# Performance work log

Hardware: AMD Instinct MI355X
Metric: run time of the kernel (lower is better)

Reference implementation:

```python
import jax, jax.numpy as jnp
import numpy as np

NEG_SLOPE = 0.01  # nn.LeakyReLU default
N_NODES = 38332
POI_LEN = 38333
CAT_LEN = 400
POI_DIM = 300
CAT_DIM = 100
GCN_CH = 64
GCN_LAYERS = 5
N_EDGES = N_NODES * 32


def leaky(x):
    return jnp.where(x >= 0, x, NEG_SLOPE * x)


def gcn_conv(x, src, dst, W, b):
    """PyG GCNConv: add self loops + symmetric normalization.
    out = D^-1/2 (A+I) D^-1/2 X W + b, deg computed with self loops."""
    n = x.shape[0]
    h = x @ W  # [N, out]
    deg = jax.ops.segment_sum(jnp.ones_like(dst, dtype=h.dtype), dst, num_segments=n) + 1.0
    dinv = jax.lax.rsqrt(deg)  # deg >= 1 always (self loop)
    norm = dinv[src] * dinv[dst]  # [E]
    agg = jax.ops.segment_sum(h[src] * norm[:, None], dst, num_segments=n)
    agg = agg + h * (1.0 / deg)[:, None]  # self-loop term: norm_ii = 1/deg_i
    return agg + b


def setup_inputs() -> dict:
    key = jax.random.key(0)
    ks = jax.random.split(key, 16)
    poi_ids = jax.random.randint(ks[0], (N_NODES, 1), 0, POI_LEN).astype(jnp.float32)
    cat_ids = jax.random.randint(ks[1], (N_NODES, 1), 0, CAT_LEN).astype(jnp.float32)
    feats = jax.random.normal(ks[2], (N_NODES, 3), dtype=jnp.float32)
    x = jnp.concatenate([poi_ids, cat_ids, feats], axis=1)  # [N,5]
    edge_index = jax.random.randint(ks[3], (2, N_EDGES), 0, N_NODES, dtype=jnp.int32)

    def glorot(k, shape):
        lim = float(np.sqrt(6.0 / (shape[0] + shape[1])))
        return jax.random.uniform(k, shape, jnp.float32, -lim, lim)

    d_in = POI_DIM + CAT_DIM + 3  # 403
    params = {
        "poi_emb": jax.random.normal(ks[4], (POI_LEN, POI_DIM), jnp.float32),
        "cat_emb": jax.random.normal(ks[5], (CAT_LEN, CAT_DIM), jnp.float32),
        "W_in": glorot(ks[6], (d_in, GCN_CH)),
        "b_in": jnp.zeros((GCN_CH,), jnp.float32),
        "gcn_Ws": jnp.stack([glorot(jax.random.fold_in(ks[7], i), (GCN_CH, GCN_CH)) for i in range(GCN_LAYERS)]),
        "gcn_bs": jnp.zeros((GCN_LAYERS, GCN_CH), jnp.float32),
        "W_out": glorot(ks[8], (GCN_CH, 1)),
        "b_out": jnp.zeros((1,), jnp.float32),
        "fc1_W": glorot(ks[9], (N_NODES, 128)),
        "fc1_b": jnp.zeros((128,), jnp.float32),
        "fc2_W": glorot(ks[10], (128, POI_LEN)),
        "fc2_b": jnpos if False else jnp.zeros((POI_LEN,), jnp.float32),
    }
    return {"x": x, "edge_index": edge_index, **params}


def reference(x, edge_index, poi_emb, cat_emb, W_in, b_in, gcn_Ws, gcn_bs, W_out, b_out, fc1_W, fc1_b, fc2_W, fc2_b):
    src, dst = edge_index[0], edge_index[1]
    poi_f = poi_emb[x[:, 0].astype(jnp.int32)]  # [N,300]
    cat_f = cat_emb[x[:, 1].astype(jnp.int32)]  # [N,100]
    feat = jnp.concatenate([poi_f, cat_f, x[:, 2:5]], axis=1)  # [N,403]
    feat = leaky(gcn_conv(feat, src, dst, W_in, b_in))
    for i in range(GCN_LAYERS):
        t = gcn_conv(feat, src, dst, gcn_Ws[i], gcn_bs[i])
        feat = leaky(t) + t  # GcnUnit: relu(temp) + temp
    feat = leaky(gcn_conv(feat, src, dst, W_out, b_out)).reshape(-1)  # [N]
    h = jax.nn.relu(feat @ fc1_W + fc1_b)
    out = jax.nn.relu(h @ fc2_W + fc2_b)  # [poi_len]
    return out
```

## Files before the change

### kernel.cpp

```cpp
#include <hip/hip_runtime.h>
#include <hip/hip_bf16.h>

#define N_NODES 38332
#define POI_LEN 38333
#define CAT_LEN 400
#define POI_DIM 300
#define CAT_DIM 100
#define N_EDGES (N_NODES * 32)
#define NEG_SLOPE 0.01f
#define B1 ((N_NODES + 127) / 128)
#define SPLIT_CHUNK 2048
#define NSPLIT ((N_EDGES + SPLIT_CHUNK - 1) / SPLIT_CHUNK)
#define PLACE_CAP 8192
#define BCAP 8192

typedef __attribute__((ext_vector_type(8))) short short8;
typedef __attribute__((ext_vector_type(4))) float f32x4;

__device__ __forceinline__ unsigned short f2bf(float f) {
  unsigned u = __float_as_uint(f);
  u += 0x7fff + ((u >> 16) & 1);
  return (unsigned short)(u >> 16);
}
__device__ __forceinline__ float bflo(unsigned u) {
  return __uint_as_float(u << 16);
}
__device__ __forceinline__ float bfhi(unsigned u) {
  return __uint_as_float(u & 0xffff0000u);
}


#define WFIN_ELEMS (13 * 2048)
#define WFGCN_ELEMS (5 * 4096)

__global__ __launch_bounds__(256) void k_prep(const float* __restrict__ W_in,
                                              const float* __restrict__ gcn_Ws,
                                              unsigned short* __restrict__ wf_in,
                                              unsigned short* __restrict__ wf_gcn,
                                              int* __restrict__ bcnt,
                                              float* __restrict__ h128) {
  int idx = blockIdx.x * 256 + threadIdx.x;
  if (idx < B1) bcnt[idx] = 0;
  if (idx < 128) h128[idx] = 0.f;
  if (idx < WFIN_ELEMS) {
    int j = idx & 7, n = (idx >> 3) & 63, q = (idx >> 9) & 3, ks = idx >> 11;
    int k = ks * 32 + q * 8 + j;
    wf_in[idx] = f2bf((k < 400) ? W_in[k * 64 + n] : 0.f);
  } else if (idx < WFIN_ELEMS + WFGCN_ELEMS) {
    int t = idx - WFIN_ELEMS;
    int l = t >> 12, i = t & 4095;
    int j = i & 7, n = (i >> 3) & 63, q = (i >> 9) & 3, ks = i >> 11;
    int k = ks * 32 + q * 8 + j;
    wf_gcn[t] = f2bf(gcn_Ws[(size_t)l * 4096 + k * 64 + n]);
  }
}


__global__ __launch_bounds__(256) void k_split(const int* __restrict__ src,
                                               const int* __restrict__ dst,
                                               int* __restrict__ bcnt,
                                               int* __restrict__ staging) {
  __shared__ int hist[B1];
  __shared__ int lbase[B1];
  __shared__ int lcur[B1];
  int tid = threadIdx.x;
  int base = blockIdx.x * SPLIT_CHUNK;
  int n = N_EDGES - base;
  if (n > SPLIT_CHUNK) n = SPLIT_CHUNK;
  for (int b = tid; b < B1; b += 256) {
    hist[b] = 0;
    lcur[b] = 0;
  }
  __syncthreads();
  for (int i = tid; i < n; i += 256) atomicAdd(&hist[dst[base + i] >> 7], 1);
  __syncthreads();
  for (int b = tid; b < B1; b += 256) {
    int c = hist[b];
    lbase[b] = c ? atomicAdd(&bcnt[b], c) : 0;
  }
  __syncthreads();
  for (int i = tid; i < n; i += 256) {
    int d = dst[base + i];
    int s = src[base + i];
    int b = d >> 7;
    int off = atomicAdd(&lcur[b], 1);
    staging[(size_t)b * BCAP + lbase[b] + off] = (s << 7) | (d & 127);
  }
}

__global__ __launch_bounds__(256) void k_place(const int* __restrict__ staging,
                                               const int* __restrict__ bcnt,
                                               int* __restrict__ csr_src,
                                               int2* __restrict__ rs,
                                               float* __restrict__ dinv) {
  __shared__ int lc[128];
  __shared__ int ls[256];
  __shared__ int cur[128];
  __shared__ int buf[PLACE_CAP];
  int b = blockIdx.x;
  int tid = threadIdx.x;
  int d0 = b * 128;
  int nd = N_NODES - d0;
  if (nd > 128) nd = 128;
  int cnt_b = bcnt[b];
  const int* st = staging + (size_t)b * BCAP;
  if (tid < 128) lc[tid] = 0;
  __syncthreads();
  for (int i = tid; i < cnt_b; i += 256) atomicAdd(&lc[st[i] & 127], 1);
  __syncthreads();
  int v = (tid < 128) ? lc[tid] : 0;
  ls[tid] = v;
  __syncthreads();
  for (int off = 1; off < 128; off <<= 1) {
    int t = (tid >= off) ? ls[tid - off] : 0;
    __syncthreads();
    ls[tid] += t;
    __syncthreads();
  }
  if (tid < 128) {
    int excl = ls[tid] - v;
    cur[tid] = excl;
    if (tid < nd) {
      rs[d0 + tid] = make_int2(b * BCAP + excl, v);
      dinv[d0 + tid] = 1.0f / sqrtf((float)(v + 1));
    }
  }
  __syncthreads();
  for (int i = tid; i < cnt_b; i += 256) {
    int p = st[i];
    int pos = atomicAdd(&cur[p & 127], 1);
    buf[pos] = p >> 7;
  }
  __syncthreads();
  int base = b * BCAP;
  for (int i = tid; i < cnt_b; i += 256) csr_src[base + i] = buf[i];
}


__global__ __launch_bounds__(256) void k_front(
    const float* __restrict__ x, const float* __restrict__ poi_emb,
    const float* __restrict__ cat_emb, const float* __restrict__ W_in,
    const unsigned short* __restrict__ wf_in, const float* __restrict__ dinv,
    unsigned short* __restrict__ hs) {
  constexpr int KP = 416, RS = 424, NK4 = 104;
  __shared__ unsigned short sA[16 * RS];
  __shared__ float sC[16 * 68];
  __shared__ int sPid[16], sCid[16];
  __shared__ float sX[16][3];
  int tid = threadIdx.x;
  int row0 = blockIdx.x * 16;
  if (tid < 16) {
    int row = row0 + tid;
    if (row < N_NODES) {
      sPid[tid] = (int)x[row * 5 + 0];
      sCid[tid] = (int)x[row * 5 + 1];
      sX[tid][0] = x[row * 5 + 2];
      sX[tid][1] = x[row * 5 + 3];
      sX[tid][2] = x[row * 5 + 4];
    } else {
      sPid[tid] = 0; sCid[tid] = 0;
      sX[tid][0] = sX[tid][1] = sX[tid][2] = 0.f;
    }
  }
  __syncthreads();
  for (int idx = tid; idx < 16 * NK4; idx += 256) {
    int r = idx / NK4;
    int k = (idx - r * NK4) * 4;
    ushort4 o = {0, 0, 0, 0};
    if (k < 400 && row0 + r < N_NODES) {
      float4 f;
      if (k < 300) f = *(const float4*)(poi_emb + (size_t)sPid[r] * 300 + k);
      else         f = *(const float4*)(cat_emb + (size_t)sCid[r] * 100 + (k - 300));
      o.x = f2bf(f.x); o.y = f2bf(f.y); o.z = f2bf(f.z); o.w = f2bf(f.w);
    }
    *(ushort4*)&sA[r * RS + k] = o;
  }
  __syncthreads();
  int lane = tid & 63, wv = tid >> 6;
  int c = lane & 15, q = lane >> 4, n0 = wv * 16;
  f32x4 acc = {0.f, 0.f, 0.f, 0.f};
  const unsigned short* arow = &sA[c * RS];
#pragma unroll
  for (int ks = 0; ks < KP / 32; ks++) {
    short8 af = *(const short8*)(arow + ks * 32 + q * 8);
    short8 bf = *(const short8*)(wf_in + ((size_t)((ks * 4 + q) * 64 + n0 + c)) * 8);
    acc = __builtin_amdgcn_mfma_f32_16x16x32_bf16(af, bf, acc, 0, 0, 0);
  }
#pragma unroll
  for (int r = 0; r < 4; r++) sC[(q * 4 + r) * 68 + n0 + c] = acc[r];
  __syncthreads();
  for (int idx = tid; idx < 16 * 64; idx += 256) {
    int r = idx >> 6, col = idx & 63;
    int row = row0 + r;
    if (row < N_NODES) {
      float v = sC[r * 68 + col] + sX[r][0] * W_in[400 * 64 + col] +
                sX[r][1] * W_in[401 * 64 + col] + sX[r][2] * W_in[402 * 64 + col];
      hs[(size_t)row * 64 + col] = f2bf(v * dinv[row]);
    }
  }
}


template <int MODE>
__global__ __launch_bounds__(256) void k_agg(const unsigned short* __restrict__ hs,
                                             const int2* __restrict__ rs,
                                             const int* __restrict__ csr_src,
                                             const float* __restrict__ dinv,
                                             const float* __restrict__ bias,
                                             const unsigned short* __restrict__ Wf,
                                             unsigned short* __restrict__ hs_next,
                                             const float* __restrict__ W_out,
                                             float* __restrict__ hs1) {
  __shared__ unsigned short sA[16 * 72];
  __shared__ float sC[4 * 68];
  int tid = threadIdx.x;
  int lane = tid & 63;
  int wv = tid >> 6;
  int node = blockIdx.x * 4 + wv;
  int eslot = lane >> 3;
  int ch8 = lane & 7;
  if (MODE != 2) {
    for (int i = tid; i < 216; i += 256)
      *(ushort4*)&sA[288 + i * 4] = (ushort4){0, 0, 0, 0};
  }
  int2 rr = rs[node];
  int r0 = rr.x, r1 = rr.x + rr.y;
  float4 a0 = {0.f, 0.f, 0.f, 0.f}, a1 = a0;
#define ACC8(v)                                                              \
  do {                                                                       \
    a0.x += bflo((v).x); a0.y += bfhi((v).x);                                \
    a0.z += bflo((v).y); a0.w += bfhi((v).y);                                \
    a1.x += bflo((v).z); a1.y += bfhi((v).z);                                \
    a1.z += bflo((v).w); a1.w += bfhi((v).w);                                \
  } while (0)
  int e = r0 + eslot;
  for (; e + 24 < r1; e += 32) {
    int s0 = csr_src[e];
    int s1 = csr_src[e + 8];
    int s2 = csr_src[e + 16];
    int s3 = csr_src[e + 24];
    uint4 v0 = *(const uint4*)(hs + (size_t)s0 * 64 + ch8 * 8);
    uint4 v1 = *(const uint4*)(hs + (size_t)s1 * 64 + ch8 * 8);
    uint4 v2 = *(const uint4*)(hs + (size_t)s2 * 64 + ch8 * 8);
    uint4 v3 = *(const uint4*)(hs + (size_t)s3 * 64 + ch8 * 8);
    ACC8(v0); ACC8(v1); ACC8(v2); ACC8(v3);
  }
  if (e + 8 < r1) {
    int s0 = csr_src[e];
    int s1 = csr_src[e + 8];
    uint4 v0 = *(const uint4*)(hs + (size_t)s0 * 64 + ch8 * 8);
    uint4 v1 = *(const uint4*)(hs + (size_t)s1 * 64 + ch8 * 8);
    ACC8(v0); ACC8(v1);
    e += 16;
  }
  if (e < r1) {
    int s = csr_src[e];
    uint4 v = *(const uint4*)(hs + (size_t)s * 64 + ch8 * 8);
    ACC8(v);
  }
#undef ACC8
#pragma unroll
  for (int off = 8; off <= 32; off <<= 1) {
    a0.x += __shfl_xor(a0.x, off, 64);
    a0.y += __shfl_xor(a0.y, off, 64);
    a0.z += __shfl_xor(a0.z, off, 64);
    a0.w += __shfl_xor(a0.w, off, 64);
    a1.x += __shfl_xor(a1.x, off, 64);
    a1.y += __shfl_xor(a1.y, off, 64);
    a1.z += __shfl_xor(a1.z, off, 64);
    a1.w += __shfl_xor(a1.w, off, 64);
  }
  float dn = dinv[node];
  if (lane < 8) {
    uint4 sv = *(const uint4*)(hs + (size_t)node * 64 + ch8 * 8);
    float4 bb0 = *(const float4*)(bias + ch8 * 8);
    float4 bb1 = *(const float4*)(bias + ch8 * 8 + 4);
    float4 t0, t1;
    t0.x = dn * (a0.x + bflo(sv.x)) + bb0.x;
    t0.y = dn * (a0.y + bfhi(sv.x)) + bb0.y;
    t0.z = dn * (a0.z + bflo(sv.y)) + bb0.z;
    t0.w = dn * (a0.w + bfhi(sv.y)) + bb0.w;
    t1.x = dn * (a1.x + bflo(sv.z)) + bb1.x;
    t1.y = dn * (a1.y + bfhi(sv.z)) + bb1.y;
    t1.z = dn * (a1.z + bflo(sv.w)) + bb1.z;
    t1.w = dn * (a1.w + bfhi(sv.w)) + bb1.w;
    float4 l0, l1, o0, o1;
    l0.x = (t0.x >= 0.f) ? t0.x : NEG_SLOPE * t0.x;
    l0.y = (t0.y >= 0.f) ? t0.y : NEG_SLOPE * t0.y;
    l0.z = (t0.z >= 0.f) ? t0.z : NEG_SLOPE * t0.z;
    l0.w = (t0.w >= 0.f) ? t0.w : NEG_SLOPE * t0.w;
    l1.x = (t1.x >= 0.f) ? t1.x : NEG_SLOPE * t1.x;
    l1.y = (t1.y >= 0.f) ? t1.y : NEG_SLOPE * t1.y;
    l1.z = (t1.z >= 0.f) ? t1.z : NEG_SLOPE * t1.z;
    l1.w = (t1.w >= 0.f) ? t1.w : NEG_SLOPE * t1.w;
    if (MODE == 0) {
      o0 = l0; o1 = l1;
    } else {
      o0.x = l0.x + t0.x; o0.y = l0.y + t0.y; o0.z = l0.z + t0.z; o0.w = l0.w + t0.w;
      o1.x = l1.x + t1.x; o1.y = l1.y + t1.y; o1.z = l1.z + t1.z; o1.w = l1.w + t1.w;
    }
    if (MODE == 2) {
      float4 w0 = *(const float4*)(W_out + ch8 * 8);
      float4 w1 = *(const float4*)(W_out + ch8 * 8 + 4);
      float p = o0.x * w0.x + o0.y * w0.y + o0.z * w0.z + o0.w * w0.w +
                o1.x * w1.x + o1.y * w1.y + o1.z * w1.z + o1.w * w1.w;
      p += __shfl_xor(p, 1, 64);
      p += __shfl_xor(p, 2, 64);
      p += __shfl_xor(p, 4, 64);
      if (lane == 0) hs1[node] = p * dn;
    } else {
      uint4 pk;
      pk.x = (unsigned)f2bf(o0.x) | ((unsigned)f2bf(o0.y) << 16);
      pk.y = (unsigned)f2bf(o0.z) | ((unsigned)f2bf(o0.w) << 16);
      pk.z = (unsigned)f2bf(o1.x) | ((unsigned)f2bf(o1.y) << 16);
      pk.w = (unsigned)f2bf(o1.z) | ((unsigned)f2bf(o1.w) << 16);
      *(uint4*)&sA[wv * 72 + ch8 * 8] = pk;
    }
  }
  if (MODE != 2) {
    __syncthreads();
    int c = lane & 15, q = lane >> 4, n0 = wv * 16;
    f32x4 acc = {0.f, 0.f, 0.f, 0.f};
    const unsigned short* arow = &sA[c * 72];
#pragma unroll
    for (int ks = 0; ks < 2; ks++) {
      short8 af = *(const short8*)(arow + ks * 32 + q * 8);
      short8 bf = *(const short8*)(Wf + ((size_t)((ks * 4 + q) * 64 + n0 + c)) * 8);
      acc = __builtin_amdgcn_mfma_f32_16x16x32_bf16(af, bf, acc, 0, 0, 0);
    }
    if (q == 0) {
#pragma unroll
      for (int r = 0; r < 4; r++) sC[r * 68 + n0 + c] = acc[r];
    }
    __syncthreads();
    if (tid < 128) {
      int r = tid >> 5, c2 = (tid & 31) * 2;
      int row = blockIdx.x * 4 + r;
      float dr = dinv[row];
      unsigned lo = f2bf(sC[r * 68 + c2] * dr);
      unsigned hi = f2bf(sC[r * 68 + c2 + 1] * dr);
      *(unsigned*)(hs_next + (size_t)row * 64 + c2) = lo | (hi << 16);
    }
  }
}


__global__ __launch_bounds__(256) void k_out_agg(const float* __restrict__ hs1,
                                                 const int2* __restrict__ rs,
                                                 const int* __restrict__ csr_src,
                                                 const float* __restrict__ dinv,
                                                 const float* __restrict__ b_out,
                                                 float* __restrict__ g) {
  int lane = threadIdx.x & 63;
  int w = threadIdx.x >> 6;
  int node = blockIdx.x * 4 + w;
  int2 rr = rs[node];
  int r0 = rr.x, r1 = rr.x + rr.y;
  float acc = 0.f;
  for (int e = r0 + lane; e < r1; e += 64) acc += hs1[csr_src[e]];
#pragma unroll
  for (int off = 32; off; off >>= 1) acc += __shfl_xor(acc, off, 64);
  if (lane == 0) {
    float t = dinv[node] * (acc + hs1[node]) + b_out[0];
    g[node] = (t >= 0.f) ? t : NEG_SLOPE * t;
  }
}


__global__ __launch_bounds__(128) void k_fc1(const float* __restrict__ g,
                                             const float* __restrict__ fc1_W,
                                             float* __restrict__ h128) {
  int j = threadIdx.x;
  int base = blockIdx.x * 32;
  int end = base + 32;
  if (end > N_NODES) end = N_NODES;
  float acc = 0.f;
  int i = base;
  for (; i + 4 <= end; i += 4) {
    acc += g[i + 0] * fc1_W[(size_t)(i + 0) * 128 + j];
    acc += g[i + 1] * fc1_W[(size_t)(i + 1) * 128 + j];
    acc += g[i + 2] * fc1_W[(size_t)(i + 2) * 128 + j];
    acc += g[i + 3] * fc1_W[(size_t)(i + 3) * 128 + j];
  }
  for (; i < end; i++) acc += g[i] * fc1_W[(size_t)i * 128 + j];
  atomicAdd(&h128[j], acc);
}

__global__ __launch_bounds__(256) void k_fc2(const float* __restrict__ h128raw,
                                             const float* __restrict__ fc1_b,
                                             const float* __restrict__ fc2_W,
                                             const float* __restrict__ fc2_b,
                                             float* __restrict__ out) {
  __shared__ float sh[128];
  int tid = threadIdx.x;
  if (tid < 128) {
    float v = h128raw[tid] + fc1_b[tid];
    sh[tid] = (v > 0.f) ? v : 0.f;
  }
  __syncthreads();
  int p = blockIdx.x * 256 + tid;
  if (p < POI_LEN) {
    float acc = fc2_b[p];
#pragma unroll 8
    for (int j = 0; j < 128; j++) acc += sh[j] * fc2_W[(size_t)j * POI_LEN + p];
    out[p] = (acc > 0.f) ? acc : 0.f;
  }
}


extern "C" void kernel_launch(void* const* d_in, const int* in_sizes, int n_in,
                              void* d_out, int out_size, void* d_ws, size_t ws_size,
                              hipStream_t stream) {
  const float* x       = (const float*)d_in[0];
  const int*   ei      = (const int*)d_in[1];
  const float* poi_emb = (const float*)d_in[2];
  const float* cat_emb = (const float*)d_in[3];
  const float* W_in    = (const float*)d_in[4];
  const float* b_in    = (const float*)d_in[5];
  const float* gcn_Ws  = (const float*)d_in[6];
  const float* gcn_bs  = (const float*)d_in[7];
  const float* W_out   = (const float*)d_in[8];
  const float* b_out   = (const float*)d_in[9];
  const float* fc1_W   = (const float*)d_in[10];
  const float* fc1_b   = (const float*)d_in[11];
  const float* fc2_W   = (const float*)d_in[12];
  const float* fc2_b   = (const float*)d_in[13];
  const int* src = ei;
  const int* dst = ei + N_EDGES;

  char* p = (char*)d_ws;
  auto take = [&](size_t bytes) {
    char* r = p;
    p += (bytes + 255) & ~(size_t)255;
    return r;
  };
  int2*  rs        = (int2*)take((size_t)N_NODES * 8);
  float* dinv      = (float*)take((size_t)N_NODES * 4);
  int*   bcnt      = (int*)take((size_t)B1 * 4);
  int*   csr_src   = (int*)take((size_t)B1 * BCAP * 4);
  unsigned short* hsA = (unsigned short*)take((size_t)N_NODES * 64 * 2);
  unsigned short* hsB = (unsigned short*)take((size_t)N_NODES * 64 * 2);
  float* hs1       = (float*)take((size_t)N_NODES * 4);
  float* g         = (float*)take((size_t)N_NODES * 4);
  float* h128      = (float*)take(128 * 4);
  unsigned short* wf_in  = (unsigned short*)take((size_t)WFIN_ELEMS * 2);
  unsigned short* wf_gcn = (unsigned short*)take((size_t)WFGCN_ELEMS * 2);
  int* staging = (int*)hsA;
  float* out = (float*)d_out;

  const int nb4 = N_NODES / 4;
  const int nb16 = (N_NODES + 15) / 16;

  k_prep<<<(WFIN_ELEMS + WFGCN_ELEMS + 255) / 256, 256, 0, stream>>>(
      W_in, gcn_Ws, wf_in, wf_gcn, bcnt, h128);
  k_split<<<NSPLIT, 256, 0, stream>>>(src, dst, bcnt, staging);
  k_place<<<B1, 256, 0, stream>>>(staging, bcnt, csr_src, rs, dinv);

  k_front<<<nb16, 256, 0, stream>>>(x, poi_emb, cat_emb, W_in, wf_in, dinv, hsA);

  k_agg<0><<<nb4, 256, 0, stream>>>(hsA, rs, csr_src, dinv, b_in,
                                    wf_gcn + 0 * 4096, hsB, nullptr, nullptr);
  k_agg<1><<<nb4, 256, 0, stream>>>(hsB, rs, csr_src, dinv, gcn_bs + 0 * 64,
                                    wf_gcn + 1 * 4096, hsA, nullptr, nullptr);
  k_agg<1><<<nb4, 256, 0, stream>>>(hsA, rs, csr_src, dinv, gcn_bs + 1 * 64,
                                    wf_gcn + 2 * 4096, hsB, nullptr, nullptr);
  k_agg<1><<<nb4, 256, 0, stream>>>(hsB, rs, csr_src, dinv, gcn_bs + 2 * 64,
                                    wf_gcn + 3 * 4096, hsA, nullptr, nullptr);
  k_agg<1><<<nb4, 256, 0, stream>>>(hsA, rs, csr_src, dinv, gcn_bs + 3 * 64,
                                    wf_gcn + 4 * 4096, hsB, nullptr, nullptr);
  k_agg<2><<<nb4, 256, 0, stream>>>(hsB, rs, csr_src, dinv, gcn_bs + 4 * 64,
                                    nullptr, nullptr, W_out, hs1);

  k_out_agg<<<nb4, 256, 0, stream>>>(hs1, rs, csr_src, dinv, b_out, g);
  k_fc1<<<(N_NODES + 31) / 32, 128, 0, stream>>>(g, fc1_W, h128);
  k_fc2<<<(POI_LEN + 255) / 256, 256, 0, stream>>>(h128, fc1_b, fc2_W, fc2_b, out);
}
```

Baseline: 408.2 us.

## Replace bucketed two-pass CSR build with fixed-slot per-node atomic scatter

Replaces the split/place bucket sort that built a compact CSR with a single kernel that atomically appends each edge's source into a fixed 96-slot row per destination node. Degree normalisation is now computed in the front kernel from the per-node counts, and the aggregation kernels index rows by node*NSLOT with the self feature load hoisted earlier. This removes one kernel and the shared-memory histogram/scan passes, at the cost of global atomic contention, a larger sparse adjacency buffer, nondeterministic neighbour order, and a hard cap of 96 in-edges per node.

```diff
diff --git a/kernel.cpp b/kernel.cpp
--- a/kernel.cpp
+++ b/kernel.cpp
@@ -8,11 +8,7 @@
 #define CAT_DIM 100
 #define N_EDGES (N_NODES * 32)
 #define NEG_SLOPE 0.01f
-#define B1 ((N_NODES + 127) / 128)
-#define SPLIT_CHUNK 2048
-#define NSPLIT ((N_EDGES + SPLIT_CHUNK - 1) / SPLIT_CHUNK)
-#define PLACE_CAP 8192
-#define BCAP 8192
+#define NSLOT 96
 
 typedef __attribute__((ext_vector_type(8))) short short8;
 typedef __attribute__((ext_vector_type(4))) float f32x4;
@@ -28,6 +24,10 @@
 __device__ __forceinline__ float bfhi(unsigned u) {
   return __uint_as_float(u & 0xffff0000u);
 }
+__device__ __forceinline__ void acc8(float4& a0, float4& a1, uint4 v) {
+  a0.x += bflo(v.x); a0.y += bfhi(v.x); a0.z += bflo(v.y); a0.w += bfhi(v.y);
+  a1.x += bflo(v.z); a1.y += bfhi(v.z); a1.z += bflo(v.w); a1.w += bfhi(v.w);
+}
 
 
 #define WFIN_ELEMS (13 * 2048)
@@ -37,10 +37,10 @@
                                               const float* __restrict__ gcn_Ws,
                                               unsigned short* __restrict__ wf_in,
                                               unsigned short* __restrict__ wf_gcn,
-                                              int* __restrict__ bcnt,
+                                              int* __restrict__ cnt,
                                               float* __restrict__ h128) {
   int idx = blockIdx.x * 256 + threadIdx.x;
-  if (idx < B1) bcnt[idx] = 0;
+  if (idx < N_NODES) cnt[idx] = 0;
   if (idx < 128) h128[idx] = 0.f;
   if (idx < WFIN_ELEMS) {
     int j = idx & 7, n = (idx >> 3) & 63, q = (idx >> 9) & 3, ks = idx >> 11;
@@ -56,97 +56,30 @@
 }
 
 
-__global__ __launch_bounds__(256) void k_split(const int* __restrict__ src,
-                                               const int* __restrict__ dst,
-                                               int* __restrict__ bcnt,
-                                               int* __restrict__ staging) {
-  __shared__ int hist[B1];
-  __shared__ int lbase[B1];
-  __shared__ int lcur[B1];
-  int tid = threadIdx.x;
-  int base = blockIdx.x * SPLIT_CHUNK;
-  int n = N_EDGES - base;
-  if (n > SPLIT_CHUNK) n = SPLIT_CHUNK;
-  for (int b = tid; b < B1; b += 256) {
-    hist[b] = 0;
-    lcur[b] = 0;
-  }
-  __syncthreads();
-  for (int i = tid; i < n; i += 256) atomicAdd(&hist[dst[base + i] >> 7], 1);
-  __syncthreads();
-  for (int b = tid; b < B1; b += 256) {
-    int c = hist[b];
-    lbase[b] = c ? atomicAdd(&bcnt[b], c) : 0;
-  }
-  __syncthreads();
-  for (int i = tid; i < n; i += 256) {
-    int d = dst[base + i];
-    int s = src[base + i];
-    int b = d >> 7;
-    int off = atomicAdd(&lcur[b], 1);
-    staging[(size_t)b * BCAP + lbase[b] + off] = (s << 7) | (d & 127);
-  }
-}
-
-__global__ __launch_bounds__(256) void k_place(const int* __restrict__ staging,
-                                               const int* __restrict__ bcnt,
-                                               int* __restrict__ csr_src,
-                                               int2* __restrict__ rs,
-                                               float* __restrict__ dinv) {
-  __shared__ int lc[128];
-  __shared__ int ls[256];
-  __shared__ int cur[128];
-  __shared__ int buf[PLACE_CAP];
-  int b = blockIdx.x;
-  int tid = threadIdx.x;
-  int d0 = b * 128;
-  int nd = N_NODES - d0;
-  if (nd > 128) nd = 128;
-  int cnt_b = bcnt[b];
-  const int* st = staging + (size_t)b * BCAP;
-  if (tid < 128) lc[tid] = 0;
-  __syncthreads();
-  for (int i = tid; i < cnt_b; i += 256) atomicAdd(&lc[st[i] & 127], 1);
-  __syncthreads();
-  int v = (tid < 128) ? lc[tid] : 0;
-  ls[tid] = v;
-  __syncthreads();
-  for (int off = 1; off < 128; off <<= 1) {
-    int t = (tid >= off) ? ls[tid - off] : 0;
-    __syncthreads();
-    ls[tid] += t;
-    __syncthreads();
-  }
-  if (tid < 128) {
-    int excl = ls[tid] - v;
-    cur[tid] = excl;
-    if (tid < nd) {
-      rs[d0 + tid] = make_int2(b * BCAP + excl, v);
-      dinv[d0 + tid] = 1.0f / sqrtf((float)(v + 1));
-    }
-  }
-  __syncthreads();
-  for (int i = tid; i < cnt_b; i += 256) {
-    int p = st[i];
-    int pos = atomicAdd(&cur[p & 127], 1);
-    buf[pos] = p >> 7;
-  }
-  __syncthreads();
-  int base = b * BCAP;
-  for (int i = tid; i < cnt_b; i += 256) csr_src[base + i] = buf[i];
+__global__ __launch_bounds__(256) void k_scatter(const int* __restrict__ src,
+                                                 const int* __restrict__ dst,
+                                                 int* __restrict__ cnt,
+                                                 int* __restrict__ csr) {
+  int i = blockIdx.x * 256 + threadIdx.x;
+  if (i >= N_EDGES) return;
+  int s = src[i];
+  int d = dst[i];
+  int pos = atomicAdd(&cnt[d], 1);
+  csr[(size_t)d * NSLOT + pos] = s;
 }
 
 
 __global__ __launch_bounds__(256) void k_front(
     const float* __restrict__ x, const float* __restrict__ poi_emb,
     const float* __restrict__ cat_emb, const float* __restrict__ W_in,
-    const unsigned short* __restrict__ wf_in, const float* __restrict__ dinv,
-    unsigned short* __restrict__ hs) {
-  constexpr int KP = 416, RS = 424, NK4 = 104;
+    const unsigned short* __restrict__ wf_in, const int* __restrict__ cnt,
+    float* __restrict__ dinv, unsigned short* __restrict__ hs) {
+  constexpr int RS = 424;
   __shared__ unsigned short sA[16 * RS];
   __shared__ float sC[16 * 68];
   __shared__ int sPid[16], sCid[16];
   __shared__ float sX[16][3];
+  __shared__ float sDinv[16];
   int tid = threadIdx.x;
   int row0 = blockIdx.x * 16;
   if (tid < 16) {
@@ -157,15 +90,19 @@
       sX[tid][0] = x[row * 5 + 2];
       sX[tid][1] = x[row * 5 + 3];
       sX[tid][2] = x[row * 5 + 4];
+      float dn = 1.0f / sqrtf((float)(cnt[row] + 1));
+      sDinv[tid] = dn;
+      dinv[row] = dn;
     } else {
       sPid[tid] = 0; sCid[tid] = 0;
       sX[tid][0] = sX[tid][1] = sX[tid][2] = 0.f;
+      sDinv[tid] = 0.f;
     }
   }
   __syncthreads();
-  for (int idx = tid; idx < 16 * NK4; idx += 256) {
-    int r = idx / NK4;
-    int k = (idx - r * NK4) * 4;
+  for (int idx = tid; idx < 16 * 104; idx += 256) {
+    int r = idx / 104;
+    int k = (idx - r * 104) * 4;
     ushort4 o = {0, 0, 0, 0};
     if (k < 400 && row0 + r < N_NODES) {
       float4 f;
@@ -181,7 +118,7 @@
   f32x4 acc = {0.f, 0.f, 0.f, 0.f};
   const unsigned short* arow = &sA[c * RS];
 #pragma unroll
-  for (int ks = 0; ks < KP / 32; ks++) {
+  for (int ks = 0; ks < 13; ks++) {
     short8 af = *(const short8*)(arow + ks * 32 + q * 8);
     short8 bf = *(const short8*)(wf_in + ((size_t)((ks * 4 + q) * 64 + n0 + c)) * 8);
     acc = __builtin_amdgcn_mfma_f32_16x16x32_bf16(af, bf, acc, 0, 0, 0);
@@ -195,7 +132,7 @@
     if (row < N_NODES) {
       float v = sC[r * 68 + col] + sX[r][0] * W_in[400 * 64 + col] +
                 sX[r][1] * W_in[401 * 64 + col] + sX[r][2] * W_in[402 * 64 + col];
-      hs[(size_t)row * 64 + col] = f2bf(v * dinv[row]);
+      hs[(size_t)row * 64 + col] = f2bf(v * sDinv[r]);
     }
   }
 }
@@ -203,8 +140,8 @@
 
 template <int MODE>
 __global__ __launch_bounds__(256) void k_agg(const unsigned short* __restrict__ hs,
-                                             const int2* __restrict__ rs,
-                                             const int* __restrict__ csr_src,
+                                             const int* __restrict__ cnt,
+                                             const int* __restrict__ csr,
                                              const float* __restrict__ dinv,
                                              const float* __restrict__ bias,
                                              const unsigned short* __restrict__ Wf,
@@ -223,42 +160,37 @@
     for (int i = tid; i < 216; i += 256)
       *(ushort4*)&sA[288 + i * 4] = (ushort4){0, 0, 0, 0};
   }
-  int2 rr = rs[node];
-  int r0 = rr.x, r1 = rr.x + rr.y;
+  int deg = cnt[node];
+  float dn = dinv[node];
+  const int* crow = csr + (size_t)node * NSLOT;
+  uint4 sv = {0, 0, 0, 0};
+  if (lane < 8) sv = *(const uint4*)(hs + (size_t)node * 64 + ch8 * 8);
   float4 a0 = {0.f, 0.f, 0.f, 0.f}, a1 = a0;
-#define ACC8(v)                                                              \
-  do {                                                                       \
-    a0.x += bflo((v).x); a0.y += bfhi((v).x);                                \
-    a0.z += bflo((v).y); a0.w += bfhi((v).y);                                \
-    a1.x += bflo((v).z); a1.y += bfhi((v).z);                                \
-    a1.z += bflo((v).w); a1.w += bfhi((v).w);                                \
-  } while (0)
-  int e = r0 + eslot;
-  for (; e + 24 < r1; e += 32) {
-    int s0 = csr_src[e];
-    int s1 = csr_src[e + 8];
-    int s2 = csr_src[e + 16];
-    int s3 = csr_src[e + 24];
+  int j = eslot;
+  for (; j + 24 < deg; j += 32) {
+    int s0 = crow[j];
+    int s1 = crow[j + 8];
+    int s2 = crow[j + 16];
+    int s3 = crow[j + 24];
     uint4 v0 = *(const uint4*)(hs + (size_t)s0 * 64 + ch8 * 8);
     uint4 v1 = *(const uint4*)(hs + (size_t)s1 * 64 + ch8 * 8);
     uint4 v2 = *(const uint4*)(hs + (size_t)s2 * 64 + ch8 * 8);
     uint4 v3 = *(const uint4*)(hs + (size_t)s3 * 64 + ch8 * 8);
-    ACC8(v0); ACC8(v1); ACC8(v2); ACC8(v3);
-  }
-  if (e + 8 < r1) {
-    int s0 = csr_src[e];
-    int s1 = csr_src[e + 8];
+    acc8(a0, a1, v0); acc8(a0, a1, v1); acc8(a0, a1, v2); acc8(a0, a1, v3);
+  }
+  if (j + 8 < deg) {
+    int s0 = crow[j];
+    int s1 = crow[j + 8];
     uint4 v0 = *(const uint4*)(hs + (size_t)s0 * 64 + ch8 * 8);
     uint4 v1 = *(const uint4*)(hs + (size_t)s1 * 64 + ch8 * 8);
-    ACC8(v0); ACC8(v1);
-    e += 16;
-  }
-  if (e < r1) {
-    int s = csr_src[e];
+    acc8(a0, a1, v0); acc8(a0, a1, v1);
+    j += 16;
+  }
+  if (j < deg) {
+    int s = crow[j];
     uint4 v = *(const uint4*)(hs + (size_t)s * 64 + ch8 * 8);
-    ACC8(v);
-  }
-#undef ACC8
+    acc8(a0, a1, v);
+  }
 #pragma unroll
   for (int off = 8; off <= 32; off <<= 1) {
     a0.x += __shfl_xor(a0.x, off, 64);
@@ -270,9 +202,7 @@
     a1.z += __shfl_xor(a1.z, off, 64);
     a1.w += __shfl_xor(a1.w, off, 64);
   }
-  float dn = dinv[node];
   if (lane < 8) {
-    uint4 sv = *(const uint4*)(hs + (size_t)node * 64 + ch8 * 8);
     float4 bb0 = *(const float4*)(bias + ch8 * 8);
     float4 bb1 = *(const float4*)(bias + ch8 * 8 + 4);
     float4 t0, t1;
@@ -346,18 +276,18 @@
 
 
 __global__ __launch_bounds__(256) void k_out_agg(const float* __restrict__ hs1,
-                                                 const int2* __restrict__ rs,
-                                                 const int* __restrict__ csr_src,
+                                                 const int* __restrict__ cnt,
+                                                 const int* __restrict__ csr,
                                                  const float* __restrict__ dinv,
                                                  const float* __restrict__ b_out,
                                                  float* __restrict__ g) {
   int lane = threadIdx.x & 63;
   int w = threadIdx.x >> 6;
   int node = blockIdx.x * 4 + w;
-  int2 rr = rs[node];
-  int r0 = rr.x, r1 = rr.x + rr.y;
+  int deg = cnt[node];
+  const int* crow = csr + (size_t)node * NSLOT;
   float acc = 0.f;
-  for (int e = r0 + lane; e < r1; e += 64) acc += hs1[csr_src[e]];
+  for (int e = lane; e < deg; e += 64) acc += hs1[crow[e]];
 #pragma unroll
   for (int off = 32; off; off >>= 1) acc += __shfl_xor(acc, off, 64);
   if (lane == 0) {
@@ -434,44 +364,42 @@
     p += (bytes + 255) & ~(size_t)255;
     return r;
   };
-  int2*  rs        = (int2*)take((size_t)N_NODES * 8);
-  float* dinv      = (float*)take((size_t)N_NODES * 4);
-  int*   bcnt      = (int*)take((size_t)B1 * 4);
-  int*   csr_src   = (int*)take((size_t)B1 * BCAP * 4);
+  int*   cnt  = (int*)take((size_t)N_NODES * 4);
+  float* dinv = (float*)take((size_t)N_NODES * 4);
+  int*   csr  = (int*)take((size_t)N_NODES * NSLOT * 4);
   unsigned short* hsA = (unsigned short*)take((size_t)N_NODES * 64 * 2);
   unsigned short* hsB = (unsigned short*)take((size_t)N_NODES * 64 * 2);
-  float* hs1       = (float*)take((size_t)N_NODES * 4);
-  float* g         = (float*)take((size_t)N_NODES * 4);
-  float* h128      = (float*)take(128 * 4);
+  float* hs1  = (float*)take((size_t)N_NODES * 4);
+  float* g    = (float*)take((size_t)N_NODES * 4);
+  float* h128 = (float*)take(128 * 4);
   unsigned short* wf_in  = (unsigned short*)take((size_t)WFIN_ELEMS * 2);
   unsigned short* wf_gcn = (unsigned short*)take((size_t)WFGCN_ELEMS * 2);
-  int* staging = (int*)hsA;
   float* out = (float*)d_out;
 
   const int nb4 = N_NODES / 4;
   const int nb16 = (N_NODES + 15) / 16;
 
   k_prep<<<(WFIN_ELEMS + WFGCN_ELEMS + 255) / 256, 256, 0, stream>>>(
-      W_in, gcn_Ws, wf_in, wf_gcn, bcnt, h128);
-  k_split<<<NSPLIT, 256, 0, stream>>>(src, dst, bcnt, staging);
-  k_place<<<B1, 256, 0, stream>>>(staging, bcnt, csr_src, rs, dinv);
-
-  k_front<<<nb16, 256, 0, stream>>>(x, poi_emb, cat_emb, W_in, wf_in, dinv, hsA);
-
-  k_agg<0><<<nb4, 256, 0, stream>>>(hsA, rs, csr_src, dinv, b_in,
+      W_in, gcn_Ws, wf_in, wf_gcn, cnt, h128);
+  k_scatter<<<(N_EDGES + 255) / 256, 256, 0, stream>>>(src, dst, cnt, csr);
+
+  k_front<<<nb16, 256, 0, stream>>>(x, poi_emb, cat_emb, W_in, wf_in, cnt,
+                                    dinv, hsA);
+
+  k_agg<0><<<nb4, 256, 0, stream>>>(hsA, cnt, csr, dinv, b_in,
                                     wf_gcn + 0 * 4096, hsB, nullptr, nullptr);
-  k_agg<1><<<nb4, 256, 0, stream>>>(hsB, rs, csr_src, dinv, gcn_bs + 0 * 64,
+  k_agg<1><<<nb4, 256, 0, stream>>>(hsB, cnt, csr, dinv, gcn_bs + 0 * 64,
                                     wf_gcn + 1 * 4096, hsA, nullptr, nullptr);
-  k_agg<1><<<nb4, 256, 0, stream>>>(hsA, rs, csr_src, dinv, gcn_bs + 1 * 64,
+  k_agg<1><<<nb4, 256, 0, stream>>>(hsA, cnt, csr, dinv, gcn_bs + 1 * 64,
                                     wf_gcn + 2 * 4096, hsB, nullptr, nullptr);
-  k_agg<1><<<nb4, 256, 0, stream>>>(hsB, rs, csr_src, dinv, gcn_bs + 2 * 64,
+  k_agg<1><<<nb4, 256, 0, stream>>>(hsB, cnt, csr, dinv, gcn_bs + 2 * 64,
                                     wf_gcn + 3 * 4096, hsA, nullptr, nullptr);
-  k_agg<1><<<nb4, 256, 0, stream>>>(hsA, rs, csr_src, dinv, gcn_bs + 3 * 64,
+  k_agg<1><<<nb4, 256, 0, stream>>>(hsA, cnt, csr, dinv, gcn_bs + 3 * 64,
                                     wf_gcn + 4 * 4096, hsB, nullptr, nullptr);
-  k_agg<2><<<nb4, 256, 0, stream>>>(hsB, rs, csr_src, dinv, gcn_bs + 4 * 64,
+  k_agg<2><<<nb4, 256, 0, stream>>>(hsB, cnt, csr, dinv, gcn_bs + 4 * 64,
                                     nullptr, nullptr, W_out, hs1);
 
-  k_out_agg<<<nb4, 256, 0, stream>>>(hs1, rs, csr_src, dinv, b_out, g);
+  k_out_agg<<<nb4, 256, 0, stream>>>(hs1, cnt, csr, dinv, b_out, g);
   k_fc1<<<(N_NODES + 31) / 32, 128, 0, stream>>>(g, fc1_W, h128);
   k_fc2<<<(POI_LEN + 255) / 256, 256, 0, stream>>>(h128, fc1_b, fc2_W, fc2_b, out);
 }
```

Result: slower. 446.8 us (+9.5%).
